# Optimization experiments

Hardware: AMD Instinct MI355X
Metric: run time of the kernel (lower is better)

Reference implementation:

```python
import jax, jax.numpy as jnp
import numpy as np

B, M, H, NLAYERS = 32768, 32, 64, 4
DIM_IN = (4 + 1) * M  # 160


def prelu(x, a):
    return jnp.where(x >= 0, x, a * x)


def setup_inputs() -> dict:
    key = jax.random.key(0)
    ks = jax.random.split(key, 10)

    x = jax.random.normal(ks[0], (B, M, 4), dtype=jnp.float32)
    pad_mask = jax.random.randint(ks[1], (B, M), 0, 2).astype(bool)

    def lin(k, fan_out, fan_in):
        bound = 1.0 / np.sqrt(fan_in)
        kw, kb = jax.random.split(k)
        W = jax.random.uniform(kw, (fan_out, fan_in), jnp.float32, -bound, bound)
        b = jax.random.uniform(kb, (fan_out,), jnp.float32, -bound, bound)
        return W, b

    W_in, b_in = lin(ks[2], H, DIM_IN)
    a_in = jnp.full((1,), 0.25, jnp.float32)  # PReLU slope

    enc_W, enc_b = [], []
    for i in range(NLAYERS):
        W, b = lin(ks[3 + i], H, H)
        enc_W.append(W)
        enc_b.append(b)
    W_enc = jnp.stack(enc_W)              # [4, 64, 64]
    b_enc = jnp.stack(enc_b)              # [4, 64]
    a_enc = jnp.full((NLAYERS, 1), 0.25, jnp.float32)

    W_out, b_out = lin(ks[8], M, H)       # [32, 64]

    return {"x": x, "pad_mask": pad_mask, "W_in": W_in, "b_in": b_in,
            "a_in": a_in, "W_enc": W_enc, "b_enc": b_enc, "a_enc": a_enc,
            "W_out": W_out, "b_out": b_out}


def reference(x, pad_mask, W_in, b_in, a_in, W_enc, b_enc, a_enc, W_out, b_out):
    # ---- FullyConnectedNetwork: learn per-satellite weights w [B, M] ----
    valid = (~pad_mask).astype(x.dtype)[..., None]          # [B, M, 1]
    feats = jnp.concatenate([x, valid], axis=-1)            # [B, M, 5]
    feats = feats.reshape(feats.shape[0], -1)               # [B, 5*M] (M == max_sats, pad is no-op)

    h = prelu(feats @ W_in.T + b_in, a_in)                  # [B, 64]
    for i in range(NLAYERS):
        h = prelu(h @ W_enc[i].T + b_enc[i], a_enc[i])
    w = h @ W_out.T + b_out                                  # [B, M]

    # ---- Weighted least squares: diag(w) applied as row-scale (same math as diag_embed + bmm) ----
    ones = jnp.ones(x.shape[:2] + (1,), dtype=x.dtype)
    A = jnp.concatenate([-x[:, :, 1:4], ones], axis=-1)      # [B, M, 4]
    r = x[:, :, 0:1]                                         # [B, M, 1]

    WA = w[:, :, None] * A                                   # [B, M, 4]
    Wr = w[:, :, None] * r                                   # [B, M, 1]

    WA_pinv = jnp.linalg.pinv(WA)                            # [B, 4, M]
    out = jnp.matmul(WA_pinv, Wr)[..., 0]                    # [B, 4]
    return out
```

## Files before the change

### kernel.cpp

```cpp
#include <hip/hip_runtime.h>
#include <cstddef>
#include <cstdint>

typedef float f32x4 __attribute__((ext_vector_type(4)));
typedef __bf16 bf16x8 __attribute__((ext_vector_type(8)));

#define MFMA_B16(a, b, c) __builtin_amdgcn_mfma_f32_16x16x32_bf16(a, b, c, 0, 0, 0)

#define OFF_L0   0u
#define OFF_WV   32768u
#define OFF_ENC  40960u
#define OFF_OUT  106496u

#define XB_OFF   0
#define AH_OFF   8192
#define AL_OFF   10240
#define WS_OFF   12288
#define SMEM_SZ  14400

__device__ __forceinline__ int xadr(int e, int b) { return (e << 9) | (b ^ ((e & 7) << 4)); }
__device__ __forceinline__ int aadr(int e, int b) { return (e << 7) | (b ^ ((e & 7) << 4)); }

__global__ __launch_bounds__(256)
void prep_frags(const float* __restrict__ W_in, const float* __restrict__ W_enc,
                const float* __restrict__ W_out, unsigned* __restrict__ P) {
  const int idx = blockIdx.x * 256 + threadIdx.x;
  if (idx >= 28672) return;
  const int t = idx & 3;
  const int lane = (idx >> 2) & 63;
  const int g = lane >> 4, c = lane & 15;
  const int j0 = t << 1;
  int pl;
  float w0, w1;
  if (idx < 8192) {
    const int rest = idx >> 8;
    pl = rest & 1;
    const int nt = (rest >> 1) & 3;
    const int kt = rest >> 3;
    const int n = 4 * c + nt;
    const int k = kt * 32 + g * 8 + j0;
    const int m = k >> 2, q = k & 3;
    w0 = W_in[n * 160 + 5 * m + q];
    w1 = W_in[n * 160 + 5 * m + q + 1];
  } else if (idx < 10240) {
    const int rest = (idx - 8192) >> 8;
    pl = rest & 1;
    const int nt = rest >> 1;
    const int n = 4 * c + nt;
    const int m = g * 8 + j0;
    w0 = W_in[n * 160 + 5 * m + 4];
    w1 = W_in[n * 160 + 5 * (m + 1) + 4];
  } else if (idx < 26624) {
    const int rel = idx - 10240;
    const int l = rel >> 12;
    const int rest = (rel & 4095) >> 8;
    pl = rest & 1;
    const int nt = (rest >> 1) & 3;
    const int kt = rest >> 3;
    const int n = 4 * c + nt;
    const int k = kt * 32 + g * 8 + j0;
    w0 = W_enc[(l * 64 + n) * 64 + k];
    w1 = W_enc[(l * 64 + n) * 64 + k + 1];
  } else {
    const int rel = idx - 26624;
    const int rest = rel >> 8;
    pl = rest & 1;
    const int nt = (rest >> 1) & 1;
    const int kt = rest >> 2;
    const int mcol = 16 * nt + c;
    const int k = kt * 32 + g * 8 + j0;
    w0 = W_out[mcol * 64 + k];
    w1 = W_out[mcol * 64 + k + 1];
  }
  unsigned short u0, u1;
  if (pl == 0) {
    u0 = __builtin_bit_cast(unsigned short, (__bf16)w0);
    u1 = __builtin_bit_cast(unsigned short, (__bf16)w1);
  } else {
    const __bf16 h0 = (__bf16)w0, h1 = (__bf16)w1;
    u0 = __builtin_bit_cast(unsigned short, (__bf16)(w0 - (float)h0));
    u1 = __builtin_bit_cast(unsigned short, (__bf16)(w1 - (float)h1));
  }
  P[idx] = (unsigned)u0 | ((unsigned)u1 << 16);
}

#define LOADG(R, base) do { \
  const char* p_ = wf + (base) + lane * 16; \
  R##0 = *(const bf16x8*)(p_); \
  R##1 = *(const bf16x8*)(p_ + 1024); \
  R##2 = *(const bf16x8*)(p_ + 2048); \
  R##3 = *(const bf16x8*)(p_ + 3072); \
  R##4 = *(const bf16x8*)(p_ + 4096); \
  R##5 = *(const bf16x8*)(p_ + 5120); \
  R##6 = *(const bf16x8*)(p_ + 6144); \
  R##7 = *(const bf16x8*)(p_ + 7168); \
} while (0)

#define TILE12(R, ah_, al_) do { \
  acc0 = MFMA_B16(ah_, R##0, acc0); acc0 = MFMA_B16(ah_, R##1, acc0); acc0 = MFMA_B16(al_, R##0, acc0); \
  acc1 = MFMA_B16(ah_, R##2, acc1); acc1 = MFMA_B16(ah_, R##3, acc1); acc1 = MFMA_B16(al_, R##2, acc1); \
  acc2 = MFMA_B16(ah_, R##4, acc2); acc2 = MFMA_B16(ah_, R##5, acc2); acc2 = MFMA_B16(al_, R##4, acc2); \
  acc3 = MFMA_B16(ah_, R##6, acc3); acc3 = MFMA_B16(ah_, R##7, acc3); acc3 = MFMA_B16(al_, R##6, acc3); \
} while (0)

#define L0STEP(R, kt) do { \
  bf16x8 ah_, al_; \
  xfrag(kt, ah_, al_); \
  TILE12(R, ah_, al_); \
} while (0)

#define WVSTEP(R) do { \
  const bf16x8 va_ = *(const bf16x8*)(smem + AL_OFF + aadr(c, g * 16)); \
  acc0 = MFMA_B16(va_, R##0, acc0); acc0 = MFMA_B16(va_, R##1, acc0); \
  acc1 = MFMA_B16(va_, R##2, acc1); acc1 = MFMA_B16(va_, R##3, acc1); \
  acc2 = MFMA_B16(va_, R##4, acc2); acc2 = MFMA_B16(va_, R##5, acc2); \
  acc3 = MFMA_B16(va_, R##6, acc3); acc3 = MFMA_B16(va_, R##7, acc3); \
} while (0)

#define ENCA(R, l) do { \
  { f32x4 t0_ = {ben[l][0], ben[l][0], ben[l][0], ben[l][0]}; acc0 = t0_; } \
  { f32x4 t1_ = {ben[l][1], ben[l][1], ben[l][1], ben[l][1]}; acc1 = t1_; } \
  { f32x4 t2_ = {ben[l][2], ben[l][2], ben[l][2], ben[l][2]}; acc2 = t2_; } \
  { f32x4 t3_ = {ben[l][3], ben[l][3], ben[l][3], ben[l][3]}; acc3 = t3_; } \
  const bf16x8 ah_ = *(const bf16x8*)(smem + AH_OFF + aadr(c, g * 16)); \
  const bf16x8 al_ = *(const bf16x8*)(smem + AL_OFF + aadr(c, g * 16)); \
  TILE12(R, ah_, al_); \
} while (0)

#define ENCB(R, l) do { \
  const bf16x8 ah_ = *(const bf16x8*)(smem + AH_OFF + aadr(c, 64 + g * 16)); \
  const bf16x8 al_ = *(const bf16x8*)(smem + AL_OFF + aadr(c, 64 + g * 16)); \
  TILE12(R, ah_, al_); \
  { f32x4 a4_[4] = {acc0, acc1, acc2, acc3}; act_store(a4_, aen[l]); } \
} while (0)

#define OUTSTEP(R) do { \
  const bf16x8 h0_ = *(const bf16x8*)(smem + AH_OFF + aadr(c, g * 16)); \
  const bf16x8 l0_ = *(const bf16x8*)(smem + AL_OFF + aadr(c, g * 16)); \
  const bf16x8 h1_ = *(const bf16x8*)(smem + AH_OFF + aadr(c, 64 + g * 16)); \
  const bf16x8 l1_ = *(const bf16x8*)(smem + AL_OFF + aadr(c, 64 + g * 16)); \
  wacc0 = MFMA_B16(h0_, R##0, wacc0); wacc0 = MFMA_B16(h0_, R##1, wacc0); wacc0 = MFMA_B16(l0_, R##0, wacc0); \
  wacc1 = MFMA_B16(h0_, R##2, wacc1); wacc1 = MFMA_B16(h0_, R##3, wacc1); wacc1 = MFMA_B16(l0_, R##2, wacc1); \
  wacc0 = MFMA_B16(h1_, R##4, wacc0); wacc0 = MFMA_B16(h1_, R##5, wacc0); wacc0 = MFMA_B16(l1_, R##4, wacc0); \
  wacc1 = MFMA_B16(h1_, R##6, wacc1); wacc1 = MFMA_B16(h1_, R##7, wacc1); wacc1 = MFMA_B16(l1_, R##6, wacc1); \
} while (0)

__global__ __launch_bounds__(64, 2)
void wls_mfma(const float* __restrict__ x, const int* __restrict__ pad,
              const float* __restrict__ b_in, const float* __restrict__ a_in,
              const float* __restrict__ b_enc, const float* __restrict__ a_enc,
              const float* __restrict__ b_out, const char* __restrict__ wf,
              float* __restrict__ out) {
  __shared__ __align__(16) unsigned char smem[SMEM_SZ];
  const int lane = threadIdx.x;
  const int g = lane >> 4, c = lane & 15;
  const int ew = blockIdx.x << 4;

  const float bin[4] = {b_in[4 * c], b_in[4 * c + 1], b_in[4 * c + 2], b_in[4 * c + 3]};
  float ben[4][4];
  #pragma unroll
  for (int l = 0; l < 4; ++l)
    #pragma unroll
    for (int nt = 0; nt < 4; ++nt) ben[l][nt] = b_enc[l * 64 + 4 * c + nt];
  const float bo[2] = {b_out[c], b_out[16 + c]};
  const float ain = a_in[0];
  const float aen[4] = {a_enc[0], a_enc[1], a_enc[2], a_enc[3]};

  {
    float4 xv[8];
    const char* src = (const char*)x + (size_t)ew * 512 + lane * 16;
    #pragma unroll
    for (int i = 0; i < 8; ++i) xv[i] = *(const float4*)(src + i * 1024);
    #pragma unroll
    for (int i = 0; i < 8; ++i) {
      const int off = i * 1024 + lane * 16;
      *(float4*)(smem + XB_OFF + xadr(off >> 9, off & 511)) = xv[i];
    }
  }
  {
    #pragma unroll
    for (int t = 0; t < 2; ++t) {
      const int el = lane >> 2;
      const int mq = (lane & 3) + (t << 2);
      const int4 pv = *(const int4*)(pad + (size_t)(ew + el) * 32 + (mq << 2));
      const unsigned ONE = 0x3F80u;
      const unsigned u0 = (pv.x ? 0u : ONE) | ((pv.y ? 0u : ONE) << 16);
      const unsigned u1 = (pv.z ? 0u : ONE) | ((pv.w ? 0u : ONE) << 16);
      *(uint2*)(smem + AL_OFF + aadr(el, mq << 3)) = make_uint2(u0, u1);
    }
  }

  auto xfrag = [&](int kt, bf16x8& ah, bf16x8& al) {
    const int b0 = kt * 128 + g * 32;
    const float4 v0 = *(const float4*)(smem + XB_OFF + xadr(c, b0));
    const float4 v1 = *(const float4*)(smem + XB_OFF + xadr(c, b0 + 16));
    const float vv[8] = {v0.x, v0.y, v0.z, v0.w, v1.x, v1.y, v1.z, v1.w};
    #pragma unroll
    for (int j = 0; j < 8; ++j) {
      const __bf16 h = (__bf16)vv[j];
      ah[j] = h;
      al[j] = (__bf16)(vv[j] - (float)h);
    }
  };
  auto act_store = [&](const f32x4* a4, float alpha) {
    #pragma unroll
    for (int r = 0; r < 4; ++r) {
      const int e = (g << 2) + r;
      unsigned hu[2], lu[2];
      #pragma unroll
      for (int q = 0; q < 2; ++q) {
        unsigned short hb[2], lb[2];
        #pragma unroll
        for (int s2 = 0; s2 < 2; ++s2) {
          float h = a4[2 * q + s2][r];
          h = (h >= 0.0f) ? h : alpha * h;
          const __bf16 hh = (__bf16)h;
          const __bf16 ll = (__bf16)(h - (float)hh);
          hb[s2] = __builtin_bit_cast(unsigned short, hh);
          lb[s2] = __builtin_bit_cast(unsigned short, ll);
        }
        hu[q] = (unsigned)hb[0] | ((unsigned)hb[1] << 16);
        lu[q] = (unsigned)lb[0] | ((unsigned)lb[1] << 16);
      }
      *(uint2*)(smem + AH_OFF + aadr(e, c * 8)) = make_uint2(hu[0], hu[1]);
      *(uint2*)(smem + AL_OFF + aadr(e, c * 8)) = make_uint2(lu[0], lu[1]);
    }
  };

  bf16x8 GA0, GA1, GA2, GA3, GA4, GA5, GA6, GA7;
  bf16x8 GB0, GB1, GB2, GB3, GB4, GB5, GB6, GB7;
  f32x4 acc0, acc1, acc2, acc3;
  {
    f32x4 t0 = {bin[0], bin[0], bin[0], bin[0]}; acc0 = t0;
    f32x4 t1 = {bin[1], bin[1], bin[1], bin[1]}; acc1 = t1;
    f32x4 t2 = {bin[2], bin[2], bin[2], bin[2]}; acc2 = t2;
    f32x4 t3 = {bin[3], bin[3], bin[3], bin[3]}; acc3 = t3;
  }

  LOADG(GA, OFF_L0 + 0);
  LOADG(GB, OFF_L0 + 8192);
  L0STEP(GA, 0);
  LOADG(GA, OFF_L0 + 16384);
  L0STEP(GB, 1);
  LOADG(GB, OFF_L0 + 24576);
  L0STEP(GA, 2);
  LOADG(GA, OFF_WV);
  L0STEP(GB, 3);
  LOADG(GB, OFF_ENC + 0);
  WVSTEP(GA);
  { f32x4 a4_[4] = {acc0, acc1, acc2, acc3}; act_store(a4_, ain); }
  LOADG(GA, OFF_ENC + 8192);
  ENCA(GB, 0);
  LOADG(GB, OFF_ENC + 16384);
  ENCB(GA, 0);
  LOADG(GA, OFF_ENC + 24576);
  ENCA(GB, 1);
  LOADG(GB, OFF_ENC + 32768);
  ENCB(GA, 1);
  LOADG(GA, OFF_ENC + 40960);
  ENCA(GB, 2);
  LOADG(GB, OFF_ENC + 49152);
  ENCB(GA, 2);
  LOADG(GA, OFF_ENC + 57344);
  ENCA(GB, 3);
  LOADG(GB, OFF_OUT);
  ENCB(GA, 3);

  f32x4 wacc0, wacc1;
  {
    f32x4 t0 = {bo[0], bo[0], bo[0], bo[0]}; wacc0 = t0;
    f32x4 t1 = {bo[1], bo[1], bo[1], bo[1]}; wacc1 = t1;
  }
  OUTSTEP(GB);
  {
    float* ws = (float*)(smem + WS_OFF);
    #pragma unroll
    for (int r = 0; r < 4; ++r) {
      ws[((g << 2) + r) * 33 + c] = wacc0[r];
      ws[((g << 2) + r) * 33 + 16 + c] = wacc1[r];
    }
  }

  {
    const int el = lane >> 2;
    const int p = lane & 3;
    const float* ws = (const float*)(smem + WS_OFF);
    float s[14];
    #pragma unroll
    for (int v = 0; v < 14; ++v) s[v] = 0.0f;
    #pragma unroll
    for (int t = 0; t < 8; ++t) {
      const int mm = (p << 3) + t;
      const float w = ws[el * 33 + mm];
      const float4 xv = *(const float4*)(smem + XB_OFF + xadr(el, mm << 4));
      const float r = xv.x;
      const float a1 = -xv.y, a2 = -xv.z, a3 = -xv.w;
      const float ww = w * w;
      const float w1 = ww * a1, w2 = ww * a2, w3 = ww * a3;
      s[0] += w1 * a1;  s[1] += w1 * a2;  s[2] += w1 * a3;  s[3] += w1;
      s[4] += w2 * a2;  s[5] += w2 * a3;  s[6] += w2;
      s[7] += w3 * a3;  s[8] += w3;
      s[9] += ww;
      s[10] += w1 * r;  s[11] += w2 * r;  s[12] += w3 * r;  s[13] += ww * r;
    }
    #pragma unroll
    for (int v = 0; v < 14; ++v) {
      s[v] += __shfl_xor(s[v], 1);
      s[v] += __shfl_xor(s[v], 2);
    }
    float Mt[4][5] = {
      {s[0], s[1], s[2], s[3], s[10]},
      {s[1], s[4], s[5], s[6], s[11]},
      {s[2], s[5], s[7], s[8], s[12]},
      {s[3], s[6], s[8], s[9], s[13]},
    };
    #pragma unroll
    for (int k = 0; k < 3; ++k) {
      const float inv = 1.0f / Mt[k][k];
      #pragma unroll
      for (int r2 = k + 1; r2 < 4; ++r2) {
        const float fk = Mt[r2][k] * inv;
        #pragma unroll
        for (int cc = k + 1; cc < 5; ++cc) Mt[r2][cc] -= fk * Mt[k][cc];
      }
    }
    const float th3 = Mt[3][4] / Mt[3][3];
    const float th2 = (Mt[2][4] - Mt[2][3] * th3) / Mt[2][2];
    const float th1 = (Mt[1][4] - Mt[1][3] * th3 - Mt[1][2] * th2) / Mt[1][1];
    const float th0 = (Mt[0][4] - Mt[0][3] * th3 - Mt[0][2] * th2 - Mt[0][1] * th1) / Mt[0][0];
    if (p == 0) {
      *(float4*)(out + (size_t)(ew + el) * 4) = make_float4(th0, th1, th2, th3);
    }
  }
}

extern "C" void kernel_launch(void* const* d_in, const int* in_sizes, int n_in,
                              void* d_out, int out_size, void* d_ws, size_t ws_size,
                              hipStream_t stream) {
  const float* x     = (const float*)d_in[0];
  const int*   pad   = (const int*)d_in[1];
  const float* W_in  = (const float*)d_in[2];
  const float* b_in  = (const float*)d_in[3];
  const float* a_in  = (const float*)d_in[4];
  const float* W_enc = (const float*)d_in[5];
  const float* b_enc = (const float*)d_in[6];
  const float* a_enc = (const float*)d_in[7];
  const float* W_out = (const float*)d_in[8];
  const float* b_out = (const float*)d_in[9];
  float* out = (float*)d_out;

  prep_frags<<<112, 256, 0, stream>>>(W_in, W_enc, W_out, (unsigned*)d_ws);
  wls_mfma<<<2048, 64, 0, stream>>>(x, pad, b_in, a_in, b_enc, a_enc, b_out,
                                    (const char*)d_ws, out);
}
```

Measured before the change: 97.93 us.

## Process 32 rows per wave and use two waves per block to reuse weight fragments

Each wave now handles two 16-row groups (32 batch rows) and issues MFMAs for both against the same weight fragments loaded from global memory, halving weight-fragment traffic per row. Blocks grow to two waves with separate LDS regions, and the grid shrinks from 2048 to 512 blocks. This raises accumulator register count and LDS use per block (57.6KB), which may reduce occupancy and leaves fewer blocks to spread across CUs.

After: 95.26 us. -2.7%, faster.

```diff
diff --git a/kernel.cpp b/kernel.cpp
--- a/kernel.cpp
+++ b/kernel.cpp
@@ -13,10 +13,11 @@
 #define OFF_OUT  106496u
 
 #define XB_OFF   0
-#define AH_OFF   8192
-#define AL_OFF   10240
-#define WS_OFF   12288
-#define SMEM_SZ  14400
+#define AH_OFF   16384
+#define AL_OFF   20480
+#define WS_OFF   24576
+#define PW       28800
+#define SMEM_SZ  57600
 
 __device__ __forceinline__ int xadr(int e, int b) { return (e << 9) | (b ^ ((e & 7) << 4)); }
 __device__ __forceinline__ int aadr(int e, int b) { return (e << 7) | (b ^ ((e & 7) << 4)); }
@@ -96,65 +97,94 @@
   R##7 = *(const bf16x8*)(p_ + 7168); \
 } while (0)
 
-#define TILE12(R, ah_, al_) do { \
-  acc0 = MFMA_B16(ah_, R##0, acc0); acc0 = MFMA_B16(ah_, R##1, acc0); acc0 = MFMA_B16(al_, R##0, acc0); \
-  acc1 = MFMA_B16(ah_, R##2, acc1); acc1 = MFMA_B16(ah_, R##3, acc1); acc1 = MFMA_B16(al_, R##2, acc1); \
-  acc2 = MFMA_B16(ah_, R##4, acc2); acc2 = MFMA_B16(ah_, R##5, acc2); acc2 = MFMA_B16(al_, R##4, acc2); \
-  acc3 = MFMA_B16(ah_, R##6, acc3); acc3 = MFMA_B16(ah_, R##7, acc3); acc3 = MFMA_B16(al_, R##6, acc3); \
+#define TILE12X(R, ah_, al_, q0, q1, q2, q3) do { \
+  q0 = MFMA_B16(ah_, R##0, q0); q0 = MFMA_B16(ah_, R##1, q0); q0 = MFMA_B16(al_, R##0, q0); \
+  q1 = MFMA_B16(ah_, R##2, q1); q1 = MFMA_B16(ah_, R##3, q1); q1 = MFMA_B16(al_, R##2, q1); \
+  q2 = MFMA_B16(ah_, R##4, q2); q2 = MFMA_B16(ah_, R##5, q2); q2 = MFMA_B16(al_, R##4, q2); \
+  q3 = MFMA_B16(ah_, R##6, q3); q3 = MFMA_B16(ah_, R##7, q3); q3 = MFMA_B16(al_, R##6, q3); \
 } while (0)
 
 #define L0STEP(R, kt) do { \
-  bf16x8 ah_, al_; \
-  xfrag(kt, ah_, al_); \
-  TILE12(R, ah_, al_); \
+  bf16x8 ahA_, alA_, ahB_, alB_; \
+  xfrag(0, kt, ahA_, alA_); \
+  xfrag(1, kt, ahB_, alB_); \
+  TILE12X(R, ahA_, alA_, accA0, accA1, accA2, accA3); \
+  TILE12X(R, ahB_, alB_, accB0, accB1, accB2, accB3); \
 } while (0)
 
 #define WVSTEP(R) do { \
-  const bf16x8 va_ = *(const bf16x8*)(smem + AL_OFF + aadr(c, g * 16)); \
-  acc0 = MFMA_B16(va_, R##0, acc0); acc0 = MFMA_B16(va_, R##1, acc0); \
-  acc1 = MFMA_B16(va_, R##2, acc1); acc1 = MFMA_B16(va_, R##3, acc1); \
-  acc2 = MFMA_B16(va_, R##4, acc2); acc2 = MFMA_B16(va_, R##5, acc2); \
-  acc3 = MFMA_B16(va_, R##6, acc3); acc3 = MFMA_B16(va_, R##7, acc3); \
+  const bf16x8 vaA_ = *(const bf16x8*)(smem + AL_OFF + aadr(c, g * 16)); \
+  const bf16x8 vaB_ = *(const bf16x8*)(smem + AL_OFF + aadr(16 + c, g * 16)); \
+  accA0 = MFMA_B16(vaA_, R##0, accA0); accA0 = MFMA_B16(vaA_, R##1, accA0); \
+  accA1 = MFMA_B16(vaA_, R##2, accA1); accA1 = MFMA_B16(vaA_, R##3, accA1); \
+  accA2 = MFMA_B16(vaA_, R##4, accA2); accA2 = MFMA_B16(vaA_, R##5, accA2); \
+  accA3 = MFMA_B16(vaA_, R##6, accA3); accA3 = MFMA_B16(vaA_, R##7, accA3); \
+  accB0 = MFMA_B16(vaB_, R##0, accB0); accB0 = MFMA_B16(vaB_, R##1, accB0); \
+  accB1 = MFMA_B16(vaB_, R##2, accB1); accB1 = MFMA_B16(vaB_, R##3, accB1); \
+  accB2 = MFMA_B16(vaB_, R##4, accB2); accB2 = MFMA_B16(vaB_, R##5, accB2); \
+  accB3 = MFMA_B16(vaB_, R##6, accB3); accB3 = MFMA_B16(vaB_, R##7, accB3); \
+} while (0)
+
+#define SETBIAS(l) do { \
+  { f32x4 t_ = {ben[l][0], ben[l][0], ben[l][0], ben[l][0]}; accA0 = t_; accB0 = t_; } \
+  { f32x4 t_ = {ben[l][1], ben[l][1], ben[l][1], ben[l][1]}; accA1 = t_; accB1 = t_; } \
+  { f32x4 t_ = {ben[l][2], ben[l][2], ben[l][2], ben[l][2]}; accA2 = t_; accB2 = t_; } \
+  { f32x4 t_ = {ben[l][3], ben[l][3], ben[l][3], ben[l][3]}; accA3 = t_; accB3 = t_; } \
 } while (0)
 
 #define ENCA(R, l) do { \
-  { f32x4 t0_ = {ben[l][0], ben[l][0], ben[l][0], ben[l][0]}; acc0 = t0_; } \
-  { f32x4 t1_ = {ben[l][1], ben[l][1], ben[l][1], ben[l][1]}; acc1 = t1_; } \
-  { f32x4 t2_ = {ben[l][2], ben[l][2], ben[l][2], ben[l][2]}; acc2 = t2_; } \
-  { f32x4 t3_ = {ben[l][3], ben[l][3], ben[l][3], ben[l][3]}; acc3 = t3_; } \
-  const bf16x8 ah_ = *(const bf16x8*)(smem + AH_OFF + aadr(c, g * 16)); \
-  const bf16x8 al_ = *(const bf16x8*)(smem + AL_OFF + aadr(c, g * 16)); \
-  TILE12(R, ah_, al_); \
+  SETBIAS(l); \
+  const bf16x8 ahA_ = *(const bf16x8*)(smem + AH_OFF + aadr(c, g * 16)); \
+  const bf16x8 alA_ = *(const bf16x8*)(smem + AL_OFF + aadr(c, g * 16)); \
+  const bf16x8 ahB_ = *(const bf16x8*)(smem + AH_OFF + aadr(16 + c, g * 16)); \
+  const bf16x8 alB_ = *(const bf16x8*)(smem + AL_OFF + aadr(16 + c, g * 16)); \
+  TILE12X(R, ahA_, alA_, accA0, accA1, accA2, accA3); \
+  TILE12X(R, ahB_, alB_, accB0, accB1, accB2, accB3); \
 } while (0)
 
 #define ENCB(R, l) do { \
-  const bf16x8 ah_ = *(const bf16x8*)(smem + AH_OFF + aadr(c, 64 + g * 16)); \
-  const bf16x8 al_ = *(const bf16x8*)(smem + AL_OFF + aadr(c, 64 + g * 16)); \
-  TILE12(R, ah_, al_); \
-  { f32x4 a4_[4] = {acc0, acc1, acc2, acc3}; act_store(a4_, aen[l]); } \
+  const bf16x8 ahA_ = *(const bf16x8*)(smem + AH_OFF + aadr(c, 64 + g * 16)); \
+  const bf16x8 alA_ = *(const bf16x8*)(smem + AL_OFF + aadr(c, 64 + g * 16)); \
+  const bf16x8 ahB_ = *(const bf16x8*)(smem + AH_OFF + aadr(16 + c, 64 + g * 16)); \
+  const bf16x8 alB_ = *(const bf16x8*)(smem + AL_OFF + aadr(16 + c, 64 + g * 16)); \
+  TILE12X(R, ahA_, alA_, accA0, accA1, accA2, accA3); \
+  TILE12X(R, ahB_, alB_, accB0, accB1, accB2, accB3); \
+  { f32x4 a4_[4] = {accA0, accA1, accA2, accA3}; act_store(0, a4_, aen[l]); } \
+  { f32x4 a4_[4] = {accB0, accB1, accB2, accB3}; act_store(1, a4_, aen[l]); } \
 } while (0)
 
 #define OUTSTEP(R) do { \
-  const bf16x8 h0_ = *(const bf16x8*)(smem + AH_OFF + aadr(c, g * 16)); \
-  const bf16x8 l0_ = *(const bf16x8*)(smem + AL_OFF + aadr(c, g * 16)); \
-  const bf16x8 h1_ = *(const bf16x8*)(smem + AH_OFF + aadr(c, 64 + g * 16)); \
-  const bf16x8 l1_ = *(const bf16x8*)(smem + AL_OFF + aadr(c, 64 + g * 16)); \
-  wacc0 = MFMA_B16(h0_, R##0, wacc0); wacc0 = MFMA_B16(h0_, R##1, wacc0); wacc0 = MFMA_B16(l0_, R##0, wacc0); \
-  wacc1 = MFMA_B16(h0_, R##2, wacc1); wacc1 = MFMA_B16(h0_, R##3, wacc1); wacc1 = MFMA_B16(l0_, R##2, wacc1); \
-  wacc0 = MFMA_B16(h1_, R##4, wacc0); wacc0 = MFMA_B16(h1_, R##5, wacc0); wacc0 = MFMA_B16(l1_, R##4, wacc0); \
-  wacc1 = MFMA_B16(h1_, R##6, wacc1); wacc1 = MFMA_B16(h1_, R##7, wacc1); wacc1 = MFMA_B16(l1_, R##6, wacc1); \
-} while (0)
-
-__global__ __launch_bounds__(64, 2)
+  const bf16x8 h0A_ = *(const bf16x8*)(smem + AH_OFF + aadr(c, g * 16)); \
+  const bf16x8 l0A_ = *(const bf16x8*)(smem + AL_OFF + aadr(c, g * 16)); \
+  const bf16x8 h1A_ = *(const bf16x8*)(smem + AH_OFF + aadr(c, 64 + g * 16)); \
+  const bf16x8 l1A_ = *(const bf16x8*)(smem + AL_OFF + aadr(c, 64 + g * 16)); \
+  waccA0 = MFMA_B16(h0A_, R##0, waccA0); waccA0 = MFMA_B16(h0A_, R##1, waccA0); waccA0 = MFMA_B16(l0A_, R##0, waccA0); \
+  waccA1 = MFMA_B16(h0A_, R##2, waccA1); waccA1 = MFMA_B16(h0A_, R##3, waccA1); waccA1 = MFMA_B16(l0A_, R##2, waccA1); \
+  waccA0 = MFMA_B16(h1A_, R##4, waccA0); waccA0 = MFMA_B16(h1A_, R##5, waccA0); waccA0 = MFMA_B16(l1A_, R##4, waccA0); \
+  waccA1 = MFMA_B16(h1A_, R##6, waccA1); waccA1 = MFMA_B16(h1A_, R##7, waccA1); waccA1 = MFMA_B16(l1A_, R##6, waccA1); \
+  const bf16x8 h0B_ = *(const bf16x8*)(smem + AH_OFF + aadr(16 + c, g * 16)); \
+  const bf16x8 l0B_ = *(const bf16x8*)(smem + AL_OFF + aadr(16 + c, g * 16)); \
+  const bf16x8 h1B_ = *(const bf16x8*)(smem + AH_OFF + aadr(16 + c, 64 + g * 16)); \
+  const bf16x8 l1B_ = *(const bf16x8*)(smem + AL_OFF + aadr(16 + c, 64 + g * 16)); \
+  waccB0 = MFMA_B16(h0B_, R##0, waccB0); waccB0 = MFMA_B16(h0B_, R##1, waccB0); waccB0 = MFMA_B16(l0B_, R##0, waccB0); \
+  waccB1 = MFMA_B16(h0B_, R##2, waccB1); waccB1 = MFMA_B16(h0B_, R##3, waccB1); waccB1 = MFMA_B16(l0B_, R##2, waccB1); \
+  waccB0 = MFMA_B16(h1B_, R##4, waccB0); waccB0 = MFMA_B16(h1B_, R##5, waccB0); waccB0 = MFMA_B16(l1B_, R##4, waccB0); \
+  waccB1 = MFMA_B16(h1B_, R##6, waccB1); waccB1 = MFMA_B16(h1B_, R##7, waccB1); waccB1 = MFMA_B16(l1B_, R##6, waccB1); \
+} while (0)
+
+__global__ __launch_bounds__(128, 2)
 void wls_mfma(const float* __restrict__ x, const int* __restrict__ pad,
               const float* __restrict__ b_in, const float* __restrict__ a_in,
               const float* __restrict__ b_enc, const float* __restrict__ a_enc,
               const float* __restrict__ b_out, const char* __restrict__ wf,
               float* __restrict__ out) {
-  __shared__ __align__(16) unsigned char smem[SMEM_SZ];
-  const int lane = threadIdx.x;
+  __shared__ __align__(16) unsigned char smem_all[SMEM_SZ];
+  const int tid = threadIdx.x;
+  const int wv = tid >> 6;
+  const int lane = tid & 63;
   const int g = lane >> 4, c = lane & 15;
-  const int ew = blockIdx.x << 4;
+  unsigned char* smem = smem_all + wv * PW;
+  const int ew = (blockIdx.x << 6) + (wv << 5);
 
   const float bin[4] = {b_in[4 * c], b_in[4 * c + 1], b_in[4 * c + 2], b_in[4 * c + 3]};
   float ben[4][4];
@@ -166,34 +196,34 @@
   const float ain = a_in[0];
   const float aen[4] = {a_enc[0], a_enc[1], a_enc[2], a_enc[3]};
 
-  {
+  #pragma unroll
+  for (int half = 0; half < 2; ++half) {
     float4 xv[8];
-    const char* src = (const char*)x + (size_t)ew * 512 + lane * 16;
+    const char* src = (const char*)x + (size_t)ew * 512 + half * 8192 + lane * 16;
     #pragma unroll
     for (int i = 0; i < 8; ++i) xv[i] = *(const float4*)(src + i * 1024);
     #pragma unroll
     for (int i = 0; i < 8; ++i) {
-      const int off = i * 1024 + lane * 16;
+      const int off = half * 8192 + i * 1024 + lane * 16;
       *(float4*)(smem + XB_OFF + xadr(off >> 9, off & 511)) = xv[i];
     }
   }
-  {
-    #pragma unroll
-    for (int t = 0; t < 2; ++t) {
-      const int el = lane >> 2;
-      const int mq = (lane & 3) + (t << 2);
-      const int4 pv = *(const int4*)(pad + (size_t)(ew + el) * 32 + (mq << 2));
-      const unsigned ONE = 0x3F80u;
-      const unsigned u0 = (pv.x ? 0u : ONE) | ((pv.y ? 0u : ONE) << 16);
-      const unsigned u1 = (pv.z ? 0u : ONE) | ((pv.w ? 0u : ONE) << 16);
-      *(uint2*)(smem + AL_OFF + aadr(el, mq << 3)) = make_uint2(u0, u1);
-    }
-  }
-
-  auto xfrag = [&](int kt, bf16x8& ah, bf16x8& al) {
+  #pragma unroll
+  for (int t = 0; t < 4; ++t) {
+    const int el = (t << 3) + (lane >> 3);
+    const int mq = lane & 7;
+    const int4 pv = *(const int4*)(pad + (size_t)(ew + el) * 32 + (mq << 2));
+    const unsigned ONE = 0x3F80u;
+    const unsigned u0 = (pv.x ? 0u : ONE) | ((pv.y ? 0u : ONE) << 16);
+    const unsigned u1 = (pv.z ? 0u : ONE) | ((pv.w ? 0u : ONE) << 16);
+    *(uint2*)(smem + AL_OFF + aadr(el, mq << 3)) = make_uint2(u0, u1);
+  }
+
+  auto xfrag = [&](int grp, int kt, bf16x8& ah, bf16x8& al) {
+    const int e = (grp << 4) + c;
     const int b0 = kt * 128 + g * 32;
-    const float4 v0 = *(const float4*)(smem + XB_OFF + xadr(c, b0));
-    const float4 v1 = *(const float4*)(smem + XB_OFF + xadr(c, b0 + 16));
+    const float4 v0 = *(const float4*)(smem + XB_OFF + xadr(e, b0));
+    const float4 v1 = *(const float4*)(smem + XB_OFF + xadr(e, b0 + 16));
     const float vv[8] = {v0.x, v0.y, v0.z, v0.w, v1.x, v1.y, v1.z, v1.w};
     #pragma unroll
     for (int j = 0; j < 8; ++j) {
@@ -202,10 +232,10 @@
       al[j] = (__bf16)(vv[j] - (float)h);
     }
   };
-  auto act_store = [&](const f32x4* a4, float alpha) {
+  auto act_store = [&](int grp, const f32x4* a4, float alpha) {
     #pragma unroll
     for (int r = 0; r < 4; ++r) {
-      const int e = (g << 2) + r;
+      const int e = (grp << 4) + (g << 2) + r;
       unsigned hu[2], lu[2];
       #pragma unroll
       for (int q = 0; q < 2; ++q) {
@@ -229,12 +259,12 @@
 
   bf16x8 GA0, GA1, GA2, GA3, GA4, GA5, GA6, GA7;
   bf16x8 GB0, GB1, GB2, GB3, GB4, GB5, GB6, GB7;
-  f32x4 acc0, acc1, acc2, acc3;
+  f32x4 accA0, accA1, accA2, accA3, accB0, accB1, accB2, accB3;
   {
-    f32x4 t0 = {bin[0], bin[0], bin[0], bin[0]}; acc0 = t0;
-    f32x4 t1 = {bin[1], bin[1], bin[1], bin[1]}; acc1 = t1;
-    f32x4 t2 = {bin[2], bin[2], bin[2], bin[2]}; acc2 = t2;
-    f32x4 t3 = {bin[3], bin[3], bin[3], bin[3]}; acc3 = t3;
+    f32x4 t0 = {bin[0], bin[0], bin[0], bin[0]}; accA0 = t0; accB0 = t0;
+    f32x4 t1 = {bin[1], bin[1], bin[1], bin[1]}; accA1 = t1; accB1 = t1;
+    f32x4 t2 = {bin[2], bin[2], bin[2], bin[2]}; accA2 = t2; accB2 = t2;
+    f32x4 t3 = {bin[3], bin[3], bin[3], bin[3]}; accA3 = t3; accB3 = t3;
   }
 
   LOADG(GA, OFF_L0 + 0);
@@ -248,7 +278,8 @@
   L0STEP(GB, 3);
   LOADG(GB, OFF_ENC + 0);
   WVSTEP(GA);
-  { f32x4 a4_[4] = {acc0, acc1, acc2, acc3}; act_store(a4_, ain); }
+  { f32x4 a4_[4] = {accA0, accA1, accA2, accA3}; act_store(0, a4_, ain); }
+  { f32x4 a4_[4] = {accB0, accB1, accB2, accB3}; act_store(1, a4_, ain); }
   LOADG(GA, OFF_ENC + 8192);
   ENCA(GB, 0);
   LOADG(GB, OFF_ENC + 16384);
@@ -266,23 +297,26 @@
   LOADG(GB, OFF_OUT);
   ENCB(GA, 3);
 
-  f32x4 wacc0, wacc1;
+  f32x4 waccA0, waccA1, waccB0, waccB1;
   {
-    f32x4 t0 = {bo[0], bo[0], bo[0], bo[0]}; wacc0 = t0;
-    f32x4 t1 = {bo[1], bo[1], bo[1], bo[1]}; wacc1 = t1;
+    f32x4 t0 = {bo[0], bo[0], bo[0], bo[0]}; waccA0 = t0; waccB0 = t0;
+    f32x4 t1 = {bo[1], bo[1], bo[1], bo[1]}; waccA1 = t1; waccB1 = t1;
   }
   OUTSTEP(GB);
   {
     float* ws = (float*)(smem + WS_OFF);
     #pragma unroll
     for (int r = 0; r < 4; ++r) {
-      ws[((g << 2) + r) * 33 + c] = wacc0[r];
-      ws[((g << 2) + r) * 33 + 16 + c] = wacc1[r];
-    }
-  }
-
-  {
-    const int el = lane >> 2;
+      ws[((g << 2) + r) * 33 + c] = waccA0[r];
+      ws[((g << 2) + r) * 33 + 16 + c] = waccA1[r];
+      ws[(16 + (g << 2) + r) * 33 + c] = waccB0[r];
+      ws[(16 + (g << 2) + r) * 33 + 16 + c] = waccB1[r];
+    }
+  }
+
+  #pragma unroll
+  for (int it = 0; it < 2; ++it) {
+    const int el = (it << 4) + (lane >> 2);
     const int p = lane & 3;
     const float* ws = (const float*)(smem + WS_OFF);
     float s[14];
@@ -350,6 +384,6 @@
   float* out = (float*)d_out;
 
   prep_frags<<<112, 256, 0, stream>>>(W_in, W_enc, W_out, (unsigned*)d_ws);
-  wls_mfma<<<2048, 64, 0, stream>>>(x, pad, b_in, a_in, b_enc, a_enc, b_out,
+  wls_mfma<<<512, 128, 0, stream>>>(x, pad, b_in, a_in, b_enc, a_enc, b_out,
                                     (const char*)d_ws, out);
 }
```
